# Performance work log

Hardware: AMD Instinct MI355X
Metric: run time of the kernel (lower is better)

The kernel has to match this reference:

```python
import jax, jax.numpy as jnp
import numpy as np
from jax import lax

DIM = 256
HEADS = 8
DIM_HEAD = 64
INNER = HEADS * DIM_HEAD  # 512
K = 3
PAD = K // 2
KV_STRIDE = 2
SCALE = DIM_HEAD ** -0.5
BN_EPS = 1e-5


def _dw_block(x, w_dw, g, b, m, v, w_pw, stride):
    """depthwise conv -> batchnorm (eval) -> 1x1 conv. x: [B,C,H,W]."""
    c = x.shape[1]
    h = lax.conv_general_dilated(
        x, w_dw, window_strides=(stride, stride),
        padding=[(PAD, PAD), (PAD, PAD)],
        feature_group_count=c,
        dimension_numbers=('NCHW', 'OIHW', 'NCHW'))
    inv = lax.rsqrt(v + BN_EPS)
    h = (h - m[None, :, None, None]) * (g * inv)[None, :, None, None] + b[None, :, None, None]
    return jnp.einsum('oc,bchw->bohw', w_pw, h)


def _heads_flat(t):
    # [B, h*d, H, W] -> [B, h, d, H*W]
    B, hd, H, W = t.shape
    return t.reshape(B, HEADS, DIM_HEAD, H * W)


def _cross_attn(q, k, v, Hq, Wq):
    # q: [B,h,d,i], k/v: [B,h,d,j]
    dots = jnp.einsum('bhdi,bhdj->bhij', q, k) * SCALE
    attn = jax.nn.softmax(dots, axis=-1)
    out = jnp.einsum('bhij,bhdj->bhdi', attn, v)
    B = q.shape[0]
    return out.reshape(B, INNER, Hq, Wq)


def _forward(x, y, q_dw_w, q_bn_gamma, q_bn_beta, q_bn_mean, q_bn_var, q_pw_w,
             kv_dw_w, kv_bn_gamma, kv_bn_beta, kv_bn_mean, kv_bn_var, kv_pw_w,
             out_w, out_b):
    B, _, Hx, Wx = x.shape
    _, _, Hy, Wy = y.shape

    qx = _heads_flat(_dw_block(x, q_dw_w, q_bn_gamma, q_bn_beta, q_bn_mean, q_bn_var, q_pw_w, 1))
    kvx = _dw_block(x, kv_dw_w, kv_bn_gamma, kv_bn_beta, kv_bn_mean, kv_bn_var, kv_pw_w, KV_STRIDE)
    kx, vx = map(_heads_flat, jnp.split(kvx, 2, axis=1))

    qy = _heads_flat(_dw_block(y, q_dw_w, q_bn_gamma, q_bn_beta, q_bn_mean, q_bn_var, q_pw_w, 1))
    kvy = _dw_block(y, kv_dw_w, kv_bn_gamma, kv_bn_beta, kv_bn_mean, kv_bn_var, kv_pw_w, KV_STRIDE)
    ky, vy = map(_heads_flat, jnp.split(kvy, 2, axis=1))

    outx = _cross_attn(qx, ky, vy, Hx, Wx)   # x queries attend to y keys/values
    outy = _cross_attn(qy, kx, vx, Hy, Wy)   # y queries attend to x keys/values

    def proj(o):
        return jnp.einsum('oc,bchw->bohw', out_w, o) + out_b[None, :, None, None]

    return proj(outx), proj(outy)


def setup_inputs() -> dict:
    key = jax.random.key(0)
    ks = jax.random.split(key, 8)
    B, H, W = 8, 32, 32
    return {
        'x': jax.random.normal(ks[0], (B, DIM, H, W), jnp.float32),
        'y': jax.random.normal(ks[1], (B, DIM, H, W), jnp.float32),
        'q_dw_w': jax.random.normal(ks[2], (DIM, 1, K, K), jnp.float32) * 0.1,
        'q_bn_gamma': jnp.ones((DIM,), jnp.float32),
        'q_bn_beta': jnp.zeros((DIM,), jnp.float32),
        'q_bn_mean': jnp.zeros((DIM,), jnp.float32),
        'q_bn_var': jnp.ones((DIM,), jnp.float32),
        'q_pw_w': jax.random.normal(ks[3], (INNER, DIM), jnp.float32) * (DIM ** -0.5),
        'kv_dw_w': jax.random.normal(ks[4], (DIM, 1, K, K), jnp.float32) * 0.1,
        'kv_bn_gamma': jnp.ones((DIM,), jnp.float32),
        'kv_bn_beta': jnp.zeros((DIM,), jnp.float32),
        'kv_bn_mean': jnp.zeros((DIM,), jnp.float32),
        'kv_bn_var': jnp.ones((DIM,), jnp.float32),
        'kv_pw_w': jax.random.normal(ks[5], (2 * INNER, DIM), jnp.float32) * (DIM ** -0.5),
        'out_w': jax.random.normal(ks[6], (DIM, INNER), jnp.float32) * (INNER ** -0.5),
        'out_b': jnp.zeros((DIM,), jnp.float32),
    }


def reference(x, y, q_dw_w, q_bn_gamma, q_bn_beta, q_bn_mean, q_bn_var, q_pw_w,
              kv_dw_w, kv_bn_gamma, kv_bn_beta, kv_bn_mean, kv_bn_var, kv_pw_w,
              out_w, out_b):
    return _forward(x, y, q_dw_w, q_bn_gamma, q_bn_beta, q_bn_mean, q_bn_var, q_pw_w,
                    kv_dw_w, kv_bn_gamma, kv_bn_beta, kv_bn_mean, kv_bn_var, kv_pw_w,
                    out_w, out_b)
```

## Files before the change

kernel.cpp:

```cpp
#include <hip/hip_runtime.h>

#define BN_EPS 1e-5f
#define ATT_SCALE 0.125f

typedef _Float16 half_t;
typedef _Float16 half8 __attribute__((ext_vector_type(8)));
typedef _Float16 half4 __attribute__((ext_vector_type(4)));
typedef float f32x4 __attribute__((ext_vector_type(4)));

__device__ __forceinline__ void gll16(const void* g, void* l) {
    __builtin_amdgcn_global_load_lds((const __attribute__((address_space(1))) void*)g,
                                     (__attribute__((address_space(3))) void*)l, 16, 0, 0);
}

__device__ void prep_body(
    int o, int c,
    const float* qg, const float* qb, const float* qm, const float* qv, const float* qpw,
    const float* kg, const float* kbt, const float* km, const float* kvv, const float* kvpw,
    const float* outw,
    half_t* wq, half_t* wkv, half_t* wout, float* bq, float* bkv, float* red)
{
    if (o >= 1536) {
        int ro = o - 1536;
        #pragma unroll
        for (int ci = 0; ci < 2; ++ci) {
            int cc = ci * 256 + c;
            float wv = outw[(size_t)ro * 512 + cc];
            half_t hh = (half_t)wv;
            wout[(size_t)ro * 1024 + cc]       = hh;
            wout[(size_t)ro * 1024 + 512 + cc] = (half_t)(wv - (float)hh);
        }
        return;
    }
    const float *g, *b, *m, *v, *w; half_t* we; float* be;
    if (o < 512) {
        g = qg; b = qb; m = qm; v = qv;
        w = qpw + (size_t)o * 256; we = wq + (size_t)o * 512; be = bq + o;
    } else {
        int ro = o - 512;
        g = kg; b = kbt; m = km; v = kvv;
        w = kvpw + (size_t)ro * 256; we = wkv + (size_t)ro * 512; be = bkv + ro;
    }
    float s  = g[c] * rsqrtf(v[c] + BN_EPS);
    float tt = b[c] - m[c] * s;
    float wv = w[c];
    float wsv = wv * s;
    half_t hh = (half_t)wsv;
    we[c]       = hh;
    we[256 + c] = (half_t)(wsv - (float)hh);
    float partial = wv * tt;
    #pragma unroll
    for (int off = 32; off > 0; off >>= 1)
        partial += __shfl_down(partial, off, 64);
    if ((c & 63) == 0) red[c >> 6] = partial;
    __syncthreads();
    if (c == 0) *be = red[0] + red[1] + red[2] + red[3];
}

__device__ void dw_body(
    int rp, int img, float* sin,
    const float* x, const float* y,
    const float* qdw, const float* kvdw,
    half_t* qB, half_t* kvB)
{
    const float* in = (img < 8) ? x + (size_t)img * 256 * 1024
                                : y + (size_t)(img - 8) * 256 * 1024;
    int t = threadIdx.x;
    int ch = t & 63, cg = t >> 6;
    int r0 = 2 * rp - 1;
    #pragma unroll
    for (int u = t; u < 1024; u += 256) {
        int c = u >> 4, row = (u >> 2) & 3, pi = u & 3;
        sin[c * 148 + row * 36 + (pi < 2 ? pi : 32 + pi)] = 0.f;
    }
    for (int cc = 0; cc < 4; ++cc) {
        __syncthreads();
        #pragma unroll
        for (int ii = 0; ii < 8; ++ii) {
            int u = ii * 256 + t;
            int sch = u >> 5, row = (u >> 3) & 3, seg = u & 7;
            int gr = r0 + row;
            float4 v4 = {0.f, 0.f, 0.f, 0.f};
            if (gr >= 0 && gr < 32)
                v4 = *(const float4*)(in + (size_t)(cc * 64 + sch) * 1024 + gr * 32 + seg * 4);
            float* d = &sin[sch * 148 + row * 36 + 2 + seg * 4];
            d[0] = v4.x; d[1] = v4.y; d[2] = v4.z; d[3] = v4.w;
        }
        __syncthreads();
        int gch = cc * 64 + ch;
        float wq9[9], wk9[9];
        #pragma unroll
        for (int i = 0; i < 9; ++i) { wq9[i] = qdw[gch * 9 + i]; wk9[i] = kvdw[gch * 9 + i]; }
        float rowv[4][12];
        const float* base = &sin[ch * 148];
        #pragma unroll
        for (int rr = 0; rr < 4; ++rr) {
            *(float4*)&rowv[rr][0] = *(const float4*)(base + rr * 36 + cg * 8);
            *(float4*)&rowv[rr][4] = *(const float4*)(base + rr * 36 + cg * 8 + 4);
            *(float4*)&rowv[rr][8] = *(const float4*)(base + rr * 36 + cg * 8 + 8);
        }
        #pragma unroll
        for (int r = 0; r < 2; ++r) {
            #pragma unroll
            for (int c8 = 0; c8 < 8; ++c8) {
                float acc = 0.f;
                #pragma unroll
                for (int dr = 0; dr < 3; ++dr)
                    #pragma unroll
                    for (int dc = 0; dc < 3; ++dc)
                        acc += wq9[dr * 3 + dc] * rowv[r + dr][c8 + dc + 1];
                half_t hh = (half_t)acc;
                size_t p = (size_t)img * 1024 + (2 * rp + r) * 32 + cg * 8 + c8;
                qB[p * 512 + gch]       = hh;
                qB[p * 512 + 256 + gch] = (half_t)(acc - (float)hh);
            }
        }
        #pragma unroll
        for (int c4 = 0; c4 < 4; ++c4) {
            float acc = 0.f;
            #pragma unroll
            for (int dr = 0; dr < 3; ++dr)
                #pragma unroll
                for (int dc = 0; dc < 3; ++dc)
                    acc += wk9[dr * 3 + dc] * rowv[dr][2 * c4 + dc + 1];
            half_t hh = (half_t)acc;
            size_t p = (size_t)img * 256 + rp * 16 + cg * 4 + c4;
            kvB[p * 512 + gch]       = hh;
            kvB[p * 512 + 256 + gch] = (half_t)(acc - (float)hh);
        }
    }
}

__global__ __launch_bounds__(256) void prep_dw_kernel(
    const float* __restrict__ x, const float* __restrict__ y,
    const float* __restrict__ qdw, const float* __restrict__ kvdw,
    const float* __restrict__ qg, const float* __restrict__ qb,
    const float* __restrict__ qm, const float* __restrict__ qv,
    const float* __restrict__ qpw,
    const float* __restrict__ kg, const float* __restrict__ kbt,
    const float* __restrict__ km, const float* __restrict__ kvv,
    const float* __restrict__ kvpw,
    const float* __restrict__ outw,
    half_t* __restrict__ wq, half_t* __restrict__ wkv, half_t* __restrict__ wout,
    float* __restrict__ bq, float* __restrict__ bkv,
    half_t* __restrict__ qB, half_t* __restrict__ kvB)
{
    __shared__ __align__(16) float smem[64 * 148];
    int bx = blockIdx.x;
    if (bx < 256)
        dw_body(bx & 15, bx >> 4, smem, x, y, qdw, kvdw, qB, kvB);
    else
        prep_body(bx - 256, threadIdx.x, qg, qb, qm, qv, qpw,
                  kg, kbt, km, kvv, kvpw, outw, wq, wkv, wout, bq, bkv, smem);
}

template<int MT, int NT, int WGM, int WGN, int NTHR, int MODE>
__device__ __forceinline__ void gemm_worker(
    char* lds, const half_t* Ab, const half_t* Bb,
    void* outBuf, const float* bias,
    int K, int NPX, int img, int m0, int n0, float scale)
{
    constexpr int TM = WGM * MT * 16, TN = WGN * NT * 16;
    constexpr int BUF = (TM + TN) * 128;
    int t = threadIdx.x, w = t >> 6, lane = t & 63, quad = lane >> 4, l15 = lane & 15;
    int wm = w % WGM, wn = w / WGM;
    f32x4 acc[MT][NT] = {};
    const int NC = K / 32;

    auto stage = [&](int kh, int p) {
        char* Ah = lds + p * BUF;
        char* Al = Ah + TM * 64;
        char* Bh = Ah + TM * 128;
        char* Bl = Bh + TN * 64;
        #pragma unroll
        for (int ii = 0; ii < TM * 4 / NTHR; ++ii) {
            int u = ii * NTHR + t;
            int mt = u >> 6, q = (u >> 4) & 3, r = u & 15;
            const half_t* g = Ab + (size_t)(mt * 16 + r) * (2 * K) + kh + q * 8;
            gll16(g,     Ah + (u & ~63) * 16);
            gll16(g + K, Al + (u & ~63) * 16);
        }
        #pragma unroll
        for (int ii = 0; ii < TN * 4 / NTHR; ++ii) {
            int u = ii * NTHR + t;
            int nt = u >> 6, q = (u >> 4) & 3, r = u & 15;
            const half_t* g = Bb + (size_t)(nt * 16 + r) * (2 * K) + kh + q * 8;
            gll16(g,     Bh + (u & ~63) * 16);
            gll16(g + K, Bl + (u & ~63) * 16);
        }
    };

    stage(0, 0);
    for (int kc = 0; kc < NC; ++kc) {
        __syncthreads();
        if (kc + 1 < NC) stage((kc + 1) * 32, (kc + 1) & 1);
        char* Ah = lds + (kc & 1) * BUF;
        char* Al = Ah + TM * 64;
        char* Bh = Ah + TM * 128;
        char* Bl = Bh + TN * 64;
        half8 afh[MT], afl[MT];
        #pragma unroll
        for (int mi = 0; mi < MT; ++mi) {
            afh[mi] = *(half8*)(Ah + (wm * MT + mi) * 1024 + lane * 16);
            afl[mi] = *(half8*)(Al + (wm * MT + mi) * 1024 + lane * 16);
        }
        #pragma unroll
        for (int ni = 0; ni < NT; ++ni) {
            half8 bh = *(half8*)(Bh + (wn * NT + ni) * 1024 + lane * 16);
            half8 bl = *(half8*)(Bl + (wn * NT + ni) * 1024 + lane * 16);
            #pragma unroll
            for (int mi = 0; mi < MT; ++mi) {
                acc[mi][ni] = __builtin_amdgcn_mfma_f32_16x16x32_f16(afh[mi], bh, acc[mi][ni], 0, 0, 0);
                acc[mi][ni] = __builtin_amdgcn_mfma_f32_16x16x32_f16(afh[mi], bl, acc[mi][ni], 0, 0, 0);
                acc[mi][ni] = __builtin_amdgcn_mfma_f32_16x16x32_f16(afl[mi], bh, acc[mi][ni], 0, 0, 0);
            }
        }
    }

    if (MODE == 2) {
        #pragma unroll
        for (int mi = 0; mi < MT; ++mi) {
            int mrow0 = m0 + wm * MT * 16 + mi * 16 + quad * 4;
            #pragma unroll
            for (int ni = 0; ni < NT; ++ni) {
                int col = n0 + wn * NT * 16 + ni * 16 + l15;
                f32x4 a = acc[mi][ni];
                float* op = (float*)outBuf + (size_t)img * 256 * NPX;
                #pragma unroll
                for (int r = 0; r < 4; ++r)
                    op[(size_t)(mrow0 + r) * NPX + col] = a[r] + bias[mrow0 + r];
            }
        }
    } else {
        __syncthreads();
        float* tbuf = (float*)lds;
        constexpr int TP = 40;
        #pragma unroll
        for (int qtr = 0; qtr < TM / 32; ++qtr) {
            #pragma unroll
            for (int mi = 0; mi < MT; ++mi) {
                int rowblk = wm * MT * 16 + mi * 16;
                if (rowblk >= qtr * 32 && rowblk < qtr * 32 + 32) {
                    int mloc = rowblk - qtr * 32 + quad * 4;
                    #pragma unroll
                    for (int ni = 0; ni < NT; ++ni) {
                        int nloc = wn * NT * 16 + ni * 16 + l15;
                        #pragma unroll
                        for (int r = 0; r < 4; ++r) {
                            float vv = acc[mi][ni][r];
                            if (MODE == 0) vv = (vv + bias[m0 + rowblk + quad * 4 + r]) * scale;
                            else           vv = vv + bias[n0 + nloc];
                            tbuf[nloc * TP + mloc + r] = vv;
                        }
                    }
                }
            }
            __syncthreads();
            #pragma unroll
            for (int it = 0; it < (TN * 4) / NTHR; ++it) {
                int u = it * NTHR + t;
                int n = u >> 2, mg = u & 3;
                float vv[8];
                *(float4*)&vv[0] = *(const float4*)&tbuf[n * TP + mg * 8];
                *(float4*)&vv[4] = *(const float4*)&tbuf[n * TP + mg * 8 + 4];
                half8 hv, lv;
                #pragma unroll
                for (int j = 0; j < 8; ++j) {
                    half_t hh = (half_t)vv[j];
                    hv[j] = hh; lv[j] = (half_t)(vv[j] - (float)hh);
                }
                int mglob = m0 + qtr * 32 + mg * 8;
                if (MODE == 0) {
                    int h = mglob >> 6, d0 = mglob & 63;
                    half_t* op = (half_t*)outBuf + ((size_t)(img * 8 + h) * NPX + n0 + n) * 128 + d0;
                    *(half8*)op = hv;
                    *(half8*)(op + 64) = lv;
                } else {
                    int nn = n0 + n, h = nn >> 6, d = nn & 63;
                    half_t* op = (half_t*)outBuf + ((size_t)(img * 8 + h) * 64 + d) * 512 + mglob;
                    *(half8*)op = hv;
                    *(half8*)(op + 256) = lv;
                }
            }
            __syncthreads();
        }
    }
}

__global__ __launch_bounds__(512, 4) void qkv_kernel(
    const half_t* __restrict__ wq, const half_t* __restrict__ wkv,
    const half_t* __restrict__ qB, const half_t* __restrict__ kvB,
    const float* __restrict__ bq, const float* __restrict__ bkv,
    half_t* __restrict__ qpr, half_t* __restrict__ kpr, half_t* __restrict__ vpr)
{
    __shared__ __align__(16) char lds[65536];
    int tile = blockIdx.x, img = blockIdx.z;
    if (tile < 32) {
        int m0 = (tile >> 3) * 128, n0 = (tile & 7) * 128;
        gemm_worker<2, 4, 4, 2, 512, 0>(lds,
            wq + (size_t)m0 * 512,
            qB + (size_t)img * (1024 * 512) + (size_t)n0 * 512,
            qpr, bq, 256, 1024, img, m0, n0, ATT_SCALE);
    } else if (tile < 40) {
        int tt = tile - 32;
        int m0 = (tt >> 1) * 128, n0 = (tt & 1) * 128;
        gemm_worker<2, 4, 4, 2, 512, 0>(lds,
            wkv + (size_t)m0 * 512,
            kvB + (size_t)img * (256 * 512) + (size_t)n0 * 512,
            kpr, bkv, 256, 256, img, m0, n0, 1.0f);
    } else {
        int tt = tile - 40;
        int m0 = (tt >> 2) * 128, n0 = (tt & 3) * 128;
        gemm_worker<2, 4, 4, 2, 512, 1>(lds,
            kvB + (size_t)img * (256 * 512) + (size_t)m0 * 512,
            wkv + (size_t)(512 + n0) * 512,
            vpr, bkv + 512, 256, 512, img, m0, n0, 1.0f);
    }
}

__global__ __launch_bounds__(256, 3) void out_kernel(
    const half_t* __restrict__ wout, const half_t* __restrict__ attp,
    const float* __restrict__ outb, float* __restrict__ out)
{
    __shared__ __align__(16) char lds[49152];
    int tile = blockIdx.x, img = blockIdx.z;
    int m0 = (tile >> 3) * 64, n0 = (tile & 7) * 128;
    gemm_worker<2, 4, 2, 2, 256, 2>(lds,
        wout + (size_t)m0 * 1024,
        attp + (size_t)img * (1024 * 1024) + (size_t)n0 * 1024,
        out, outb, 512, 1024, img, m0, n0, 1.0f);
}

__global__ __launch_bounds__(512, 4) void attn_fused(
    const half_t* __restrict__ qb, const half_t* __restrict__ kb,
    const half_t* __restrict__ vb, half_t* __restrict__ att)
{
    __shared__ __align__(16) char lds[65536];
    int ic = blockIdx.x, h = blockIdx.y, img = blockIdx.z;
    int partner = img ^ 8;
    int t = threadIdx.x, w = t >> 6, lane = t & 63, quad = lane >> 4, l15 = lane & 15;
    const half_t* qp = qb + ((size_t)(img * 8 + h) * 1024 + ic * 128) * 128;
    const half_t* kp = kb + (size_t)(partner * 8 + h) * 256 * 128;
    const half_t* vp = vb + (size_t)(partner * 8 + h) * 64 * 512;

    half8 qh[2], ql[2];
    #pragma unroll
    for (int kcs = 0; kcs < 2; ++kcs) {
        qh[kcs] = *(const half8*)(qp + (size_t)(w * 16 + l15) * 128 + kcs * 32 + quad * 8);
        ql[kcs] = *(const half8*)(qp + (size_t)(w * 16 + l15) * 128 + 64 + kcs * 32 + quad * 8);
    }

    #pragma unroll
    for (int ii = 0; ii < 4; ++ii) {
        int u = ii * 512 + t;
        const half_t* g = kp + (size_t)((u >> 7) * 16 + (u & 15)) * 128
                             + ((u >> 6) & 1) * 32 + ((u >> 4) & 3) * 8;
        gll16(g,      lds + (u & ~63) * 16);
        gll16(g + 64, lds + 32768 + (u & ~63) * 16);
    }
    __syncthreads();

    f32x4 sacc[16] = {};
    #pragma unroll
    for (int kcs = 0; kcs < 2; ++kcs)
        #pragma unroll
        for (int nt = 0; nt < 16; ++nt) {
            half8 bh = *(const half8*)(lds + (nt * 2 + kcs) * 1024 + lane * 16);
            half8 bl = *(const half8*)(lds + 32768 + (nt * 2 + kcs) * 1024 + lane * 16);
            sacc[nt] = __builtin_amdgcn_mfma_f32_16x16x32_f16(qh[kcs], bh, sacc[nt], 0, 0, 0);
            sacc[nt] = __builtin_amdgcn_mfma_f32_16x16x32_f16(qh[kcs], bl, sacc[nt], 0, 0, 0);
            sacc[nt] = __builtin_amdgcn_mfma_f32_16x16x32_f16(ql[kcs], bh, sacc[nt], 0, 0, 0);
        }

    #pragma unroll
    for (int r = 0; r < 4; ++r) {
        float mx = sacc[0][r];
        #pragma unroll
        for (int nt = 1; nt < 16; ++nt) mx = fmaxf(mx, sacc[nt][r]);
        #pragma unroll
        for (int off = 1; off < 16; off <<= 1) mx = fmaxf(mx, __shfl_xor(mx, off, 64));
        float sum = 0.f;
        #pragma unroll
        for (int nt = 0; nt < 16; ++nt) {
            float e = __expf(sacc[nt][r] - mx);
            sacc[nt][r] = e; sum += e;
        }
        #pragma unroll
        for (int off = 1; off < 16; off <<= 1) sum += __shfl_xor(sum, off, 64);
        float inv = 1.f / sum;
        #pragma unroll
        for (int nt = 0; nt < 16; ++nt) sacc[nt][r] *= inv;
    }
    __syncthreads();

    {
        int u = t;
        int nt = (u >> 7) & 3, kcs = (u >> 6) & 1, q = (u >> 4) & 3, r = u & 15;
        const half_t* g = vp + (size_t)(nt * 16 + r) * 512 + kcs * 32 + q * 8;
        gll16(g,       lds + (u & ~63) * 16);
        gll16(g + 256, lds + 8192 + (u & ~63) * 16);
    }

    char* Pw = lds + 32768 + w * 4096;
    f32x4 oacc[4] = {};
    for (int jc = 0; jc < 4; ++jc) {
        #pragma unroll
        for (int n4 = 0; n4 < 4; ++n4)
            #pragma unroll
            for (int r = 0; r < 4; ++r) {
                float pv = sacc[jc * 4 + n4][r];
                half_t hh = (half_t)pv;
                int row = quad * 4 + r;
                int cb = (n4 * 16 + l15) * 2;
                int off = row * 128 + (cb ^ ((row & 7) << 4));
                *(half_t*)(Pw + off) = hh;
                *(half_t*)(Pw + 2048 + off) = (half_t)(pv - (float)hh);
            }
        __syncthreads();
        if (jc < 3) {
            int u = t;
            int nt = (u >> 7) & 3, kcs = (u >> 6) & 1, q = (u >> 4) & 3, r = u & 15;
            const half_t* g = vp + (size_t)(nt * 16 + r) * 512 + (jc + 1) * 64 + kcs * 32 + q * 8;
            char* nb = lds + ((jc + 1) & 1) * 16384;
            gll16(g,       nb + (u & ~63) * 16);
            gll16(g + 256, nb + 8192 + (u & ~63) * 16);
        }
        char* vbase = lds + (jc & 1) * 16384;
        #pragma unroll
        for (int kcs = 0; kcs < 2; ++kcs) {
            int pofs = (kcs * 64 + quad * 16) ^ ((l15 & 7) << 4);
            half8 ph = *(const half8*)(Pw + l15 * 128 + pofs);
            half8 pl = *(const half8*)(Pw + 2048 + l15 * 128 + pofs);
            #pragma unroll
            for (int nt = 0; nt < 4; ++nt) {
                half8 vh = *(const half8*)(vbase + (nt * 2 + kcs) * 1024 + lane * 16);
                half8 vl = *(const half8*)(vbase + 8192 + (nt * 2 + kcs) * 1024 + lane * 16);
                oacc[nt] = __builtin_amdgcn_mfma_f32_16x16x32_f16(ph, vh, oacc[nt], 0, 0, 0);
                oacc[nt] = __builtin_amdgcn_mfma_f32_16x16x32_f16(ph, vl, oacc[nt], 0, 0, 0);
                oacc[nt] = __builtin_amdgcn_mfma_f32_16x16x32_f16(pl, vh, oacc[nt], 0, 0, 0);
            }
        }
    }

    __syncthreads();
    #pragma unroll
    for (int nt = 0; nt < 4; ++nt)
        #pragma unroll
        for (int r = 0; r < 4; ++r) {
            float vv = oacc[nt][r];
            half_t hh = (half_t)vv;
            int row = w * 16 + quad * 4 + r, col = nt * 16 + l15;
            *(half_t*)(lds + (row * 132 + col) * 2) = hh;
            *(half_t*)(lds + (row * 132 + 64 + col) * 2) = (half_t)(vv - (float)hh);
        }
    __syncthreads();
    #pragma unroll
    for (int ii = 0; ii < 4; ++ii) {
        int u = ii * 512 + t;
        int i = u >> 4, seg = (u >> 3) & 1, p8 = u & 7;
        half8 val = *(const half8*)(lds + (i * 132 + seg * 64 + p8 * 8) * 2);
        *(half8*)(att + ((size_t)img * 1024 + ic * 128 + i) * 1024 + seg * 512 + h * 64 + p8 * 8) = val;
    }
}

extern "C" void kernel_launch(void* const* d_in, const int* in_sizes, int n_in,
                              void* d_out, int out_size, void* d_ws, size_t ws_size,
                              hipStream_t stream) {
    const float* x    = (const float*)d_in[0];
    const float* y    = (const float*)d_in[1];
    const float* qdw  = (const float*)d_in[2];
    const float* qg   = (const float*)d_in[3];
    const float* qbb  = (const float*)d_in[4];
    const float* qm   = (const float*)d_in[5];
    const float* qv   = (const float*)d_in[6];
    const float* qpw  = (const float*)d_in[7];
    const float* kvdw = (const float*)d_in[8];
    const float* kg   = (const float*)d_in[9];
    const float* kb_  = (const float*)d_in[10];
    const float* km   = (const float*)d_in[11];
    const float* kvv  = (const float*)d_in[12];
    const float* kvpw = (const float*)d_in[13];
    const float* outw = (const float*)d_in[14];
    const float* outb = (const float*)d_in[15];

    char* ws = (char*)d_ws;
    half_t* wq   = (half_t*)(ws);
    half_t* wkv  = (half_t*)(ws + 524288);
    half_t* wout = (half_t*)(ws + 1572864);
    float*  bq   = (float*) (ws + 2097152);
    float*  bkv  = (float*) (ws + 2099200);
    half_t* qpr  = (half_t*)(ws + 2103296);
    half_t* kpr  = (half_t*)(ws + 35657728);
    half_t* vpr  = (half_t*)(ws + 44046336);
    half_t* qB   = (half_t*)(ws + 52434944);
    half_t* kvB  = (half_t*)(ws + 69212160);
    half_t* attp = (half_t*)(ws + 52434944);

    prep_dw_kernel<<<2048, 256, 0, stream>>>(
        x, y, qdw, kvdw, qg, qbb, qm, qv, qpw, kg, kb_, km, kvv, kvpw, outw,
        wq, wkv, wout, bq, bkv, qB, kvB);

    qkv_kernel<<<dim3(48, 1, 16), 512, 0, stream>>>(
        wq, wkv, qB, kvB, bq, bkv, qpr, kpr, vpr);

    attn_fused<<<dim3(8, 8, 16), 512, 0, stream>>>(qpr, kpr, vpr, attp);

    out_kernel<<<dim3(32, 1, 16), 256, 0, stream>>>(wout, attp, outb, (float*)d_out);
}
```

Baseline: 213.2 us.

## Defer softmax normalization, reorder attention grid, drop V double-buffering

The attention kernel now keeps only the row max after the QK pass. Exponentials are computed lazily while P is written to shared memory, and the division by the row sum moves to the output epilogue. The P tile uses a padded (stride 72) layout instead of an XOR swizzle, and V chunks are loaded single-buffered with an extra barrier per chunk instead of being prefetched. The grid is reordered so image and head are packed into blockIdx.x with query chunks in y, which changes block scheduling and cache locality; the lost V prefetch overlap adds exposed load latency.

```diff
diff --git a/kernel.cpp b/kernel.cpp
--- a/kernel.cpp
+++ b/kernel.cpp
@@ -336,7 +336,8 @@
     const half_t* __restrict__ vb, half_t* __restrict__ att)
 {
     __shared__ __align__(16) char lds[65536];
-    int ic = blockIdx.x, h = blockIdx.y, img = blockIdx.z;
+    int ic = blockIdx.y;
+    int img = blockIdx.x & 15, h = blockIdx.x >> 4;
     int partner = img ^ 8;
     int t = threadIdx.x, w = t >> 6, lane = t & 63, quad = lane >> 4, l15 = lane & 15;
     const half_t* qp = qb + ((size_t)(img * 8 + h) * 1024 + ic * 128) * 128;
@@ -372,6 +373,7 @@
             sacc[nt] = __builtin_amdgcn_mfma_f32_16x16x32_f16(ql[kcs], bh, sacc[nt], 0, 0, 0);
         }
 
+    float mrow[4];
     #pragma unroll
     for (int r = 0; r < 4; ++r) {
         float mx = sacc[0][r];
@@ -379,62 +381,41 @@
         for (int nt = 1; nt < 16; ++nt) mx = fmaxf(mx, sacc[nt][r]);
         #pragma unroll
         for (int off = 1; off < 16; off <<= 1) mx = fmaxf(mx, __shfl_xor(mx, off, 64));
-        float sum = 0.f;
-        #pragma unroll
-        for (int nt = 0; nt < 16; ++nt) {
-            float e = __expf(sacc[nt][r] - mx);
-            sacc[nt][r] = e; sum += e;
-        }
-        #pragma unroll
-        for (int off = 1; off < 16; off <<= 1) sum += __shfl_xor(sum, off, 64);
-        float inv = 1.f / sum;
-        #pragma unroll
-        for (int nt = 0; nt < 16; ++nt) sacc[nt][r] *= inv;
+        mrow[r] = mx;
     }
     __syncthreads();
 
-    {
-        int u = t;
-        int nt = (u >> 7) & 3, kcs = (u >> 6) & 1, q = (u >> 4) & 3, r = u & 15;
-        const half_t* g = vp + (size_t)(nt * 16 + r) * 512 + kcs * 32 + q * 8;
-        gll16(g,       lds + (u & ~63) * 16);
-        gll16(g + 256, lds + 8192 + (u & ~63) * 16);
-    }
-
-    char* Pw = lds + 32768 + w * 4096;
+    char* Pw = lds + 16384 + w * 4608;
     f32x4 oacc[4] = {};
+    float lsum[4] = {0.f, 0.f, 0.f, 0.f};
     for (int jc = 0; jc < 4; ++jc) {
         #pragma unroll
         for (int n4 = 0; n4 < 4; ++n4)
             #pragma unroll
             for (int r = 0; r < 4; ++r) {
-                float pv = sacc[jc * 4 + n4][r];
+                float pv = __expf(sacc[jc * 4 + n4][r] - mrow[r]);
+                lsum[r] += pv;
                 half_t hh = (half_t)pv;
-                int row = quad * 4 + r;
-                int cb = (n4 * 16 + l15) * 2;
-                int off = row * 128 + (cb ^ ((row & 7) << 4));
-                *(half_t*)(Pw + off) = hh;
-                *(half_t*)(Pw + 2048 + off) = (half_t)(pv - (float)hh);
-            }
-        __syncthreads();
-        if (jc < 3) {
-            int u = t;
-            int nt = (u >> 7) & 3, kcs = (u >> 6) & 1, q = (u >> 4) & 3, r = u & 15;
-            const half_t* g = vp + (size_t)(nt * 16 + r) * 512 + (jc + 1) * 64 + kcs * 32 + q * 8;
-            char* nb = lds + ((jc + 1) & 1) * 16384;
-            gll16(g,       nb + (u & ~63) * 16);
-            gll16(g + 256, nb + 8192 + (u & ~63) * 16);
-        }
-        char* vbase = lds + (jc & 1) * 16384;
+                int idx = ((quad * 4 + r) * 72 + n4 * 16 + l15) * 2;
+                *(half_t*)(Pw + idx) = hh;
+                *(half_t*)(Pw + 2304 + idx) = (half_t)(pv - (float)hh);
+            }
+        __syncthreads();
+        {
+            const half_t* g = vp + (size_t)(((t >> 7) & 3) * 16 + (t & 15)) * 512
+                                 + jc * 64 + ((t >> 6) & 1) * 32 + ((t >> 4) & 3) * 8;
+            gll16(g,       lds + (t & ~63) * 16);
+            gll16(g + 256, lds + 8192 + (t & ~63) * 16);
+        }
+        __syncthreads();
         #pragma unroll
         for (int kcs = 0; kcs < 2; ++kcs) {
-            int pofs = (kcs * 64 + quad * 16) ^ ((l15 & 7) << 4);
-            half8 ph = *(const half8*)(Pw + l15 * 128 + pofs);
-            half8 pl = *(const half8*)(Pw + 2048 + l15 * 128 + pofs);
+            half8 ph = *(const half8*)(Pw + (l15 * 72 + kcs * 32 + quad * 8) * 2);
+            half8 pl = *(const half8*)(Pw + 2304 + (l15 * 72 + kcs * 32 + quad * 8) * 2);
             #pragma unroll
             for (int nt = 0; nt < 4; ++nt) {
-                half8 vh = *(const half8*)(vbase + (nt * 2 + kcs) * 1024 + lane * 16);
-                half8 vl = *(const half8*)(vbase + 8192 + (nt * 2 + kcs) * 1024 + lane * 16);
+                half8 vh = *(const half8*)(lds + (nt * 2 + kcs) * 1024 + lane * 16);
+                half8 vl = *(const half8*)(lds + 8192 + (nt * 2 + kcs) * 1024 + lane * 16);
                 oacc[nt] = __builtin_amdgcn_mfma_f32_16x16x32_f16(ph, vh, oacc[nt], 0, 0, 0);
                 oacc[nt] = __builtin_amdgcn_mfma_f32_16x16x32_f16(ph, vl, oacc[nt], 0, 0, 0);
                 oacc[nt] = __builtin_amdgcn_mfma_f32_16x16x32_f16(pl, vh, oacc[nt], 0, 0, 0);
@@ -442,12 +423,21 @@
         }
     }
 
+    float inv[4];
+    #pragma unroll
+    for (int r = 0; r < 4; ++r) {
+        float s = lsum[r];
+        #pragma unroll
+        for (int off = 1; off < 16; off <<= 1) s += __shfl_xor(s, off, 64);
+        inv[r] = 1.f / s;
+    }
+
     __syncthreads();
     #pragma unroll
     for (int nt = 0; nt < 4; ++nt)
         #pragma unroll
         for (int r = 0; r < 4; ++r) {
-            float vv = oacc[nt][r];
+            float vv = oacc[nt][r] * inv[r];
             half_t hh = (half_t)vv;
             int row = w * 16 + quad * 4 + r, col = nt * 16 + l15;
             *(half_t*)(lds + (row * 132 + col) * 2) = hh;
@@ -503,7 +493,7 @@
     qkv_kernel<<<dim3(48, 1, 16), 512, 0, stream>>>(
         wq, wkv, qB, kvB, bq, bkv, qpr, kpr, vpr);
 
-    attn_fused<<<dim3(8, 8, 16), 512, 0, stream>>>(qpr, kpr, vpr, attp);
+    attn_fused<<<dim3(128, 8, 1), 512, 0, stream>>>(qpr, kpr, vpr, attp);
 
     out_kernel<<<dim3(32, 1, 16), 256, 0, stream>>>(wout, attp, outb, (float*)d_out);
 }
```

After: 208.3 us. -2.3%, faster.
